# Kernel optimization log

Measured on AMD Instinct MI355X. Metric: run time of the kernel, lower is better.

## Reference

```python
import jax, jax.numpy as jnp
import numpy as np

G = 8192          # graphs in batch
A = 5             # num_agents (nodes per graph)
N = G * A         # total nodes
IN_CH = 29
HID = 64
HEADS = 8
D = HID * HEADS   # 512, node/graph feature dim
NOPT = 4
ADIM = 3


def _lin(key, fan_in, fan_out):
    return jax.random.normal(key, (fan_in, fan_out), jnp.float32) / np.sqrt(fan_in)


def setup_inputs() -> dict:
    key = jax.random.key(0)
    ks = jax.random.split(key, 40)
    # --- graph structure: G fully-connected 5-node graphs + self loops ---
    pairs = np.array([(i, j) for i in range(A) for j in range(A) if i != j])  # [20,2]
    base = (np.arange(G)[:, None] * A)
    src = (base + pairs[None, :, 0]).reshape(-1)
    dst = (base + pairs[None, :, 1]).reshape(-1)
    # GATConv adds self loops (fill_value=0.0 for edge_attr)
    loop = np.arange(N)
    edge_src = jnp.asarray(np.concatenate([src, loop]), jnp.int32)
    edge_dst = jnp.asarray(np.concatenate([dst, loop]), jnp.int32)
    e_real = jax.random.uniform(ks[0], (src.shape[0], 1), jnp.float32)
    edge_attr = jnp.concatenate([e_real, jnp.zeros((N, 1), jnp.float32)], axis=0)
    batch_map = jnp.asarray(np.repeat(np.arange(G), A), jnp.int32)
    x = jax.random.normal(ks[1], (N, IN_CH), jnp.float32)
    sc = 1.0 / np.sqrt(HID)
    inp = dict(
        x=x, edge_attr=edge_attr, edge_src=edge_src, edge_dst=edge_dst, batch_map=batch_map,
        # conv1
        W1=_lin(ks[2], IN_CH, D), as1=jax.random.normal(ks[3], (HEADS, HID)) * sc,
        ad1=jax.random.normal(ks[4], (HEADS, HID)) * sc, We1=_lin(ks[5], 1, D),
        ae1=jax.random.normal(ks[6], (HEADS, HID)) * sc, b1=jnp.zeros((D,), jnp.float32),
        # conv2
        W2=_lin(ks[7], D, D), as2=jax.random.normal(ks[8], (HEADS, HID)) * sc,
        ad2=jax.random.normal(ks[9], (HEADS, HID)) * sc, We2=_lin(ks[10], 1, D),
        ae2=jax.random.normal(ks[11], (HEADS, HID)) * sc, b2=jnp.zeros((D,), jnp.float32),
        # policy-over-options head
        pw1=_lin(ks[12], D, 2 * HID), pb1=jnp.zeros((2 * HID,)), pw2=_lin(ks[13], 2 * HID, NOPT), pb2=jnp.zeros((NOPT,)),
        # q-options head
        qw1=_lin(ks[14], D, 2 * HID), qb1=jnp.zeros((2 * HID,)), qw2=_lin(ks[15], 2 * HID, NOPT), qb2=jnp.zeros((NOPT,)),
        # intra-option actor head (option 0), input dim = node + graph feature = 2*D
        aw1=_lin(ks[16], 2 * D, 2 * HID), ab1=jnp.zeros((2 * HID,)), aw2=_lin(ks[17], 2 * HID, 2 * ADIM), ab2=jnp.zeros((2 * ADIM,)),
        # termination head (option 0)
        tw1=_lin(ks[18], D, HID), tb1=jnp.zeros((HID,)), tw2=_lin(ks[19], HID, 1), tb2=jnp.zeros((1,)),
        action_limits=jnp.array([1.0, 1.0, 3.14159], jnp.float32),
    )
    return inp


def _gat(x, src, dst, eattr, W, a_s, a_d, We, a_e, b):
    n = x.shape[0]
    h = (x @ W).reshape(n, HEADS, HID)                      # [N,H,C]
    e = (eattr @ We).reshape(-1, HEADS, HID)                # [E,H,C]
    lg = ((h * a_s).sum(-1)[src] + (h * a_d).sum(-1)[dst]
          + (e * a_e).sum(-1))                              # [E,H]
    lg = jnp.where(lg > 0, lg, 0.2 * lg)                    # leaky_relu(0.2)
    m = jax.ops.segment_max(lg, dst, num_segments=n)
    p = jnp.exp(lg - m[dst])
    denom = jax.ops.segment_sum(p, dst, num_segments=n)[dst] + 1e-16
    alpha = p / denom                                       # scatter-softmax over dst
    out = jax.ops.segment_sum(alpha[:, :, None] * h[src], dst, num_segments=n)
    return out.reshape(n, HEADS * HID) + b


def reference(x, edge_attr, edge_src, edge_dst, batch_map,
              W1, as1, ad1, We1, ae1, b1,
              W2, as2, ad2, We2, ae2, b2,
              pw1, pb1, pw2, pb2, qw1, qb1, qw2, qb2,
              aw1, ab1, aw2, ab2, tw1, tb1, tw2, tb2, action_limits):
    h = jax.nn.relu(_gat(x, edge_src, edge_dst, edge_attr, W1, as1, ad1, We1, ae1, b1))
    h = jax.nn.relu(_gat(h, edge_src, edge_dst, edge_attr, W2, as2, ad2, We2, ae2, b2))
    # global_mean_pool
    cnt = jax.ops.segment_sum(jnp.ones((h.shape[0],), h.dtype), batch_map, num_segments=G)
    g = jax.ops.segment_sum(h, batch_map, num_segments=G) / cnt[:, None]   # [G,D]
    pi = jax.nn.relu(g @ pw1 + pb1) @ pw2 + pb2                            # [G,NOPT]
    q = jax.nn.relu(g @ qw1 + qb1) @ qw2 + qb2                             # [G,NOPT]
    term = jax.nn.sigmoid(jax.nn.relu(g @ tw1 + tb1) @ tw2 + tb2)          # [G,1]
    # per-graph first num_agents nodes == all nodes here (5 per graph)
    agent = h.reshape(G, A, D)
    comb = jnp.concatenate([agent, jnp.broadcast_to(g[:, None, :], (G, A, D))], axis=-1)
    ho = jax.nn.relu(comb @ aw1 + ab1) @ aw2 + ab2                          # [G,A,6]
    mean_raw, log_std_raw = jnp.split(ho, 2, axis=-1)
    mean = jnp.tanh(mean_raw) * action_limits                               # [G,A,3]
    std = 0.05 + jax.nn.sigmoid(log_std_raw) * 0.45 + 1e-6
    return jnp.concatenate([pi, q, term, mean.reshape(G, -1), std.reshape(G, -1)], axis=1)
```

## Files before the change

kernel.cpp:

```cpp
#include <hip/hip_runtime.h>
#include <hip/hip_bf16.h>
#include <math.h>

#define GG 8192
#define AA 5
#define NN (GG * AA)
#define DD 512

typedef unsigned short ushort_t;
typedef unsigned int uint_t;

__device__ inline float bf2f(ushort_t u) {
  union { uint_t i; float f; } c; c.i = ((uint_t)u) << 16; return c.f;
}
__device__ inline ushort_t f2bf(float f) {
  union { float f; uint_t i; } c; c.f = f;
  uint_t r = c.i + 0x7fffu + ((c.i >> 16) & 1u);
  return (ushort_t)(r >> 16);
}

using frag8 = __attribute__((ext_vector_type(8))) short;
using f32x4 = __attribute__((ext_vector_type(4))) float;

typedef __attribute__((address_space(3))) void lds_void;
typedef __attribute__((address_space(1))) const void gbl_void;
#define GLL(g, l) __builtin_amdgcn_global_load_lds((gbl_void*)(g), (lds_void*)(l), 16, 0, 0)

__device__ inline int xcd_swz(int bid, int nwg) {
  return (bid & 7) * (nwg >> 3) + (bid >> 3);
}

__global__ __launch_bounds__(256) void k_prep(
    const float* __restrict__ x, const float* __restrict__ W1,
    const float* __restrict__ W2, const float* __restrict__ pw1,
    const float* __restrict__ qw1, const float* __restrict__ tw1,
    const float* __restrict__ aw1, const float* __restrict__ pb1,
    const float* __restrict__ qb1, const float* __restrict__ tb1,
    const float* __restrict__ ab1, const float* __restrict__ We1,
    const float* __restrict__ ae1, const float* __restrict__ We2,
    const float* __restrict__ ae2, const float* __restrict__ as1,
    const float* __restrict__ ad1, const float* __restrict__ as2,
    const float* __restrict__ ad2, const float* __restrict__ pw2,
    const float* __restrict__ pb2, const float* __restrict__ qw2,
    const float* __restrict__ qb2, const float* __restrict__ tw2,
    const float* __restrict__ tb2, const float* __restrict__ aw2,
    const float* __restrict__ ab2, ushort_t* __restrict__ xpad32,
    ushort_t* __restrict__ W1T32, ushort_t* __restrict__ W2T,
    ushort_t* __restrict__ WcatT, ushort_t* __restrict__ aw1topT,
    ushort_t* __restrict__ wsc1T, ushort_t* __restrict__ wsc2T,
    float* __restrict__ bcat, float* __restrict__ sce,
    float* __restrict__ woutT, float* __restrict__ bout) {
  int b = blockIdx.x;
  int t = threadIdx.x;
  if (b < 1024) {
    int i = b * 256 + t;
    int n = i >> 9, k = i & 511;
    W2T[(size_t)n * 512 + k] = f2bf(W2[(size_t)k * 512 + n]);
    float v;
    if (n < 128)      v = pw1[(size_t)k * 128 + n];
    else if (n < 256) v = qw1[(size_t)k * 128 + (n - 128)];
    else if (n < 320) v = tw1[(size_t)k * 64 + (n - 256)];
    else if (n < 448) v = aw1[(size_t)(512 + k) * 128 + (n - 320)];
    else              v = 0.f;
    WcatT[(size_t)n * 512 + k] = f2bf(v);
    if (n < 128) aw1topT[(size_t)n * 512 + k] = f2bf(aw1[(size_t)k * 128 + n]);
    if (k == 0) {
      float bv;
      if (n < 128)      bv = pb1[n];
      else if (n < 256) bv = qb1[n - 128];
      else if (n < 320) bv = tb1[n - 256];
      else if (n < 448) bv = ab1[n - 320];
      else              bv = 0.f;
      bcat[n] = bv;
    }
    if (i < 512 * 32) {
      int nn = i >> 5, kk = i & 31;
      W1T32[i] = (kk < 29) ? f2bf(W1[(size_t)kk * 512 + nn]) : (ushort_t)0;
    }
    if (i < 16384) {
      int k2 = i & 511, srow = i >> 9;
      int nh2 = srow >> 4, s = srow & 15;
      float val = 0.f;
      if (s < 8) {
        int head = nh2 * 4 + (s >> 1);
        const float* av = ((s & 1) ? ad2 : as2) + head * 64;
        const float* wr = W2 + (size_t)k2 * 512 + head * 64;
        for (int c = 0; c < 64; ++c) val = fmaf(wr[c], av[c], val);
      }
      wsc2T[i] = f2bf(val);
    }
    if (i < 1024) {
      int k1 = i & 31, srow = i >> 5;
      int nh1 = srow >> 4, s = srow & 15;
      float val = 0.f;
      if (s < 8 && k1 < 29) {
        int head = nh1 * 4 + (s >> 1);
        const float* av = ((s & 1) ? ad1 : as1) + head * 64;
        const float* wr = W1 + (size_t)k1 * 512 + head * 64;
        for (int c = 0; c < 64; ++c) val = fmaf(wr[c], av[c], val);
      }
      wsc1T[i] = f2bf(val);
    }
    if (i < 16) {
      int h = i & 7;
      const float* Wp = (i < 8) ? We1 : We2;
      const float* ap = (i < 8) ? ae1 : ae2;
      float c = 0.f;
      for (int k2 = 0; k2 < 64; ++k2) c = fmaf(Wp[h * 64 + k2], ap[h * 64 + k2], c);
      sce[i] = c;
    }
    if (i < 5120) {
      int j = i / 40, o = i % 40;
      float wv;
      if (o < 4)       wv = pw2[j * 4 + o];
      else if (o < 8)  wv = qw2[j * 4 + (o - 4)];
      else if (o == 8) wv = (j < 64) ? tw2[j] : 0.f;
      else if (o < 24) wv = aw2[j * 6 + (o - 9) % 3];
      else if (o < 39) wv = aw2[j * 6 + 3 + (o - 24) % 3];
      else             wv = 0.f;
      woutT[i] = wv;
      if (j == 0) {
        float bv;
        if (o < 4)       bv = pb2[o];
        else if (o < 8)  bv = qb2[o - 4];
        else if (o == 8) bv = tb2[0];
        else if (o < 24) bv = ab2[(o - 9) % 3];
        else if (o < 39) bv = ab2[3 + (o - 24) % 3];
        else             bv = 0.f;
        bout[o] = bv;
      }
    }
  } else {
    int i = (b - 1024) * 256 + t;
    int n = i >> 5, k = i & 31;
    xpad32[i] = (k < 29) ? f2bf(x[(size_t)n * 29 + k]) : (ushort_t)0;
  }
}

template <int KDIM, bool POOL>
__global__ __launch_bounds__(512) void k_fused(
    const ushort_t* __restrict__ A, const ushort_t* __restrict__ BT,
    const ushort_t* __restrict__ WS, const float* __restrict__ eattr,
    const float* __restrict__ sce, const float* __restrict__ bvec,
    ushort_t* __restrict__ hout, ushort_t* __restrict__ gmean) {
  __shared__ __align__(16) char smem[54016];
  const int t = threadIdx.x;
  const int lane = t & 63;
  const int w = t >> 6;
  const int l15 = lane & 15;
  const int ko2 = ((((lane >> 4) ^ (lane & 3) ^ ((lane >> 2) & 3)) & 3) * 16);
  int lid = xcd_swz(blockIdx.x, gridDim.x);
  const int mb = lid >> 1, nh = lid & 1;
  const int m0 = mb * 80;
  const int g0 = mb * 16;
  const int n0 = nh * 256;
  const ushort_t* WSn = WS + (size_t)nh * 16 * KDIM;
  constexpr int nt = KDIM / 32;
  f32x4 acc[5][2] = {};
  f32x4 asc[5] = {};
  float* sss = (float*)(smem + 45056);
  float* ssd = (float*)(smem + 46336);
  float* sal = (float*)(smem + 47616);
#define FSTAGE(bi, kk0)                                                        \
  {                                                                            \
    char* bb_ = smem + (bi) * 16384;                                           \
    char* aa_ = smem + 32768 + (bi) * 5120;                                    \
    char* sb_ = smem + 43008 + (bi) * 1024;                                    \
    _Pragma("unroll")                                                          \
    for (int r_ = 0; r_ < 2; ++r_) {                                           \
      int c_ = t + r_ * 512; int row_ = c_ >> 2;                               \
      int sw_ = ((((c_ & 3) ^ (row_ & 3) ^ ((row_ >> 2) & 3)) & 3)) * 8;       \
      GLL(BT + (size_t)(n0 + row_) * KDIM + (kk0) + sw_, bb_ + c_ * 16);       \
    }                                                                          \
    if (t < 320) {                                                             \
      int c_ = t; int row_ = c_ >> 2;                                          \
      int sw_ = ((((c_ & 3) ^ (row_ & 3) ^ ((row_ >> 2) & 3)) & 3)) * 8;       \
      GLL(A + (size_t)(m0 + row_) * KDIM + (kk0) + sw_, aa_ + c_ * 16);        \
    } else if (t < 384) {                                                      \
      int c_ = t - 320; int row_ = c_ >> 2;                                    \
      int sw_ = ((((c_ & 3) ^ (row_ & 3) ^ ((row_ >> 2) & 3)) & 3)) * 8;       \
      GLL(WSn + (size_t)row_ * KDIM + (kk0) + sw_, sb_ + c_ * 16);             \
    }                                                                          \
  }
  FSTAGE(0, 0);
  for (int ts = 0; ts < nt; ++ts) {
    int cur = ts & 1;
    if (ts + 1 < nt) {
      FSTAGE(cur ^ 1, (ts + 1) * 32);
      if (w < 6) { asm volatile("s_waitcnt vmcnt(3)" ::: "memory"); }
      else       { asm volatile("s_waitcnt vmcnt(2)" ::: "memory"); }
    } else {
      asm volatile("s_waitcnt vmcnt(0)" ::: "memory");
    }
    __builtin_amdgcn_s_barrier();
    __builtin_amdgcn_sched_barrier(0);
    const char* bb = smem + cur * 16384;
    const char* aa = smem + 32768 + cur * 5120;
    const char* sb = smem + 43008 + cur * 1024;
    frag8 af[5], bfr[2];
#pragma unroll
    for (int mt = 0; mt < 5; ++mt)
      af[mt] = *(const frag8*)(aa + (mt * 16 + l15) * 64 + ko2);
#pragma unroll
    for (int n = 0; n < 2; ++n)
      bfr[n] = *(const frag8*)(bb + ((2 * w + n) * 16 + l15) * 64 + ko2);
    __builtin_amdgcn_s_setprio(1);
#pragma unroll
    for (int mt = 0; mt < 5; ++mt)
#pragma unroll
      for (int n = 0; n < 2; ++n)
        acc[mt][n] = __builtin_amdgcn_mfma_f32_16x16x32_bf16(af[mt], bfr[n], acc[mt][n], 0, 0, 0);
    if (w == 7) {
      frag8 sfr = *(const frag8*)(sb + l15 * 64 + ko2);
#pragma unroll
      for (int mt = 0; mt < 5; ++mt)
        asc[mt] = __builtin_amdgcn_mfma_f32_16x16x32_bf16(af[mt], sfr, asc[mt], 0, 0, 0);
    }
    __builtin_amdgcn_s_setprio(0);
    __builtin_amdgcn_sched_barrier(0);
    if (ts == nt - 1 && w == 7 && l15 < 8) {
      float* dst = (lane & 1) ? ssd : sss;
      int hd = l15 >> 1;
      int q4 = (lane >> 4) * 4;
#pragma unroll
      for (int mt = 0; mt < 5; ++mt)
#pragma unroll
        for (int r = 0; r < 4; ++r)
          dst[(mt * 16 + q4 + r) * 4 + hd] = asc[mt][r];
    }
    __builtin_amdgcn_s_barrier();
  }
#undef FSTAGE
  float* hbf = (float*)smem;
  {
    if (w < 4) {
      int q4 = (lane >> 4) * 4;
#pragma unroll
      for (int mt = 0; mt < 5; ++mt)
#pragma unroll
        for (int n = 0; n < 2; ++n) {
          int lc = w * 32 + n * 16 + l15;
#pragma unroll
          for (int r = 0; r < 4; ++r)
            hbf[(mt * 16 + q4 + r) * 132 + lc] = acc[mt][n][r];
        }
    } else if (t - 256 < 160) {
      int u = t - 256;
      int gi = u / 10, jh = u % 10;
      int j = jh >> 1, hd0 = jh & 1;
#pragma unroll
      for (int hh = 0; hh < 2; ++hh) {
        int hd = hd0 + hh * 2;
        int g = g0 + gi;
        float sdj = ssd[(gi * 5 + j) * 4 + hd];
        float ce = sce[nh * 4 + hd];
        float lg[5], mx = -1e30f;
#pragma unroll
        for (int i = 0; i < 5; ++i) {
          float l = sss[(gi * 5 + i) * 4 + hd] + sdj;
          if (i != j) l = fmaf(eattr[(size_t)g * 20 + i * 4 + (j > i ? j - 1 : j)], ce, l);
          l = l > 0.f ? l : 0.2f * l;
          lg[i] = l; mx = fmaxf(mx, l);
        }
        float s = 0.f;
#pragma unroll
        for (int i = 0; i < 5; ++i) { lg[i] = __expf(lg[i] - mx); s += lg[i]; }
        float inv = 1.f / (s + 1e-16f);
#pragma unroll
        for (int i = 0; i < 5; ++i) sal[((gi * 5 + j) * 5 + i) * 4 + hd] = lg[i] * inv;
      }
    }
  }
  __syncthreads();
#pragma unroll
  for (int half = 0; half < 2; ++half) {
    if (half == 1) {
      if (w >= 4) {
        int q4 = (lane >> 4) * 4;
#pragma unroll
        for (int mt = 0; mt < 5; ++mt)
#pragma unroll
          for (int n = 0; n < 2; ++n) {
            int lc = (w - 4) * 32 + n * 16 + l15;
#pragma unroll
            for (int r = 0; r < 4; ++r)
              hbf[(mt * 16 + q4 + r) * 132 + lc] = acc[mt][n][r];
          }
      }
      __syncthreads();
    }
    int gi = t >> 5, cq = t & 31;
    int hd = half * 2 + (cq >> 4);
    int colg = n0 + half * 128 + cq * 4;
    float hv[5][4];
#pragma unroll
    for (int i = 0; i < 5; ++i)
      *(float4*)hv[i] = *(const float4*)&hbf[(gi * 5 + i) * 132 + cq * 4];
    float4 bb4 = *(const float4*)&bvec[colg];
    float gs0 = 0.f, gs1 = 0.f, gs2 = 0.f, gs3 = 0.f;
#pragma unroll
    for (int j = 0; j < 5; ++j) {
      float o0 = bb4.x, o1 = bb4.y, o2 = bb4.z, o3 = bb4.w;
#pragma unroll
      for (int i = 0; i < 5; ++i) {
        float a = sal[((gi * 5 + j) * 5 + i) * 4 + hd];
        o0 = fmaf(a, hv[i][0], o0); o1 = fmaf(a, hv[i][1], o1);
        o2 = fmaf(a, hv[i][2], o2); o3 = fmaf(a, hv[i][3], o3);
      }
      o0 = fmaxf(o0, 0.f); o1 = fmaxf(o1, 0.f);
      o2 = fmaxf(o2, 0.f); o3 = fmaxf(o3, 0.f);
      uint2 wv_;
      wv_.x = (uint_t)f2bf(o0) | ((uint_t)f2bf(o1) << 16);
      wv_.y = (uint_t)f2bf(o2) | ((uint_t)f2bf(o3) << 16);
      *(uint2*)(hout + ((size_t)(g0 + gi) * 5 + j) * 512 + colg) = wv_;
      if (POOL) { gs0 += o0; gs1 += o1; gs2 += o2; gs3 += o3; }
    }
    if (POOL) {
      uint2 wv_;
      wv_.x = (uint_t)f2bf(gs0 * 0.2f) | ((uint_t)f2bf(gs1 * 0.2f) << 16);
      wv_.y = (uint_t)f2bf(gs2 * 0.2f) | ((uint_t)f2bf(gs3 * 0.2f) << 16);
      *(uint2*)(gmean + (size_t)(g0 + gi) * 512 + colg) = wv_;
    }
    if (half == 0) __syncthreads();
  }
}

template <int EPI>
__device__ __forceinline__ void gemm_body(
    const ushort_t* __restrict__ A, const ushort_t* __restrict__ BT,
    const float* __restrict__ bias, void* __restrict__ Cv,
    int M, int N, int K, int m0, int n0, char* lds) {
  int t = threadIdx.x;
  int lane = t & 63;
  int wv = t >> 6;
  int wr = (wv >> 1) * 64, wc = (wv & 1) * 64;
  f32x4 acc[4][4] = {};
  int ch0 = t, ch1 = t + 256;
  int row0 = ch0 >> 2, row1 = ch1 >> 2;
  int sw0 = (((ch0 & 3) ^ (row0 & 3) ^ ((row0 >> 2) & 3)) & 3) * 8;
  int sw1 = (((ch1 & 3) ^ (row1 & 3) ^ ((row1 >> 2) & 3)) & 3) * 8;
  int ko2 = ((((lane >> 4) ^ (lane & 3) ^ ((lane >> 2) & 3)) & 3) * 16);
  const int nt = K >> 5;
#define STAGE(bi, kk0)                                                         \
  {                                                                            \
    char* ab = lds + (bi) * 16384;                                             \
    GLL(A + (size_t)(m0 + row0) * K + (kk0) + sw0, ab + ch0 * 16);             \
    GLL(A + (size_t)(m0 + row1) * K + (kk0) + sw1, ab + ch1 * 16);             \
    GLL(BT + (size_t)(n0 + row0) * K + (kk0) + sw0, ab + 8192 + ch0 * 16);     \
    GLL(BT + (size_t)(n0 + row1) * K + (kk0) + sw1, ab + 8192 + ch1 * 16);     \
  }
  STAGE(0, 0);
  if (nt > 1) STAGE(1, 32);
  for (int ts = 0; ts < nt; ++ts) {
    int bi = ts % 3;
    if (ts + 2 < nt) {
      STAGE((ts + 2) % 3, (ts + 2) * 32);
      asm volatile("s_waitcnt vmcnt(8)" ::: "memory");
    } else if (ts + 1 < nt) {
      asm volatile("s_waitcnt vmcnt(4)" ::: "memory");
    } else {
      asm volatile("s_waitcnt vmcnt(0)" ::: "memory");
    }
    __builtin_amdgcn_s_barrier();
    __builtin_amdgcn_sched_barrier(0);
    const char* ab = lds + bi * 16384;
    frag8 af[4], bfr[4];
#pragma unroll
    for (int m = 0; m < 4; ++m)
      af[m] = *(const frag8*)(ab + (wr + m * 16 + (lane & 15)) * 64 + ko2);
#pragma unroll
    for (int n = 0; n < 4; ++n)
      bfr[n] = *(const frag8*)(ab + 8192 + (wc + n * 16 + (lane & 15)) * 64 + ko2);
#pragma unroll
    for (int m = 0; m < 4; ++m)
#pragma unroll
      for (int n = 0; n < 4; ++n)
        acc[m][n] = __builtin_amdgcn_mfma_f32_16x16x32_bf16(af[m], bfr[n], acc[m][n], 0, 0, 0);
    __builtin_amdgcn_sched_barrier(0);
    __builtin_amdgcn_s_barrier();
  }
#undef STAGE
  int r4 = (lane >> 4) * 4;
  int cl = lane & 15;
#pragma unroll
  for (int m = 0; m < 4; ++m) {
#pragma unroll
    for (int n = 0; n < 4; ++n) {
      int col = n0 + wc + n * 16 + cl;
      float bb = (EPI == 2) ? bias[col] : 0.f;
#pragma unroll
      for (int r = 0; r < 4; ++r) {
        int row = m0 + wr + m * 16 + r4 + r;
        float v = acc[m][n][r] + bb;
        if (EPI == 2 && col < 320) v = fmaxf(v, 0.f);
        ((float*)Cv)[(size_t)row * N + col] = v;
      }
    }
  }
}

__global__ __launch_bounds__(256) void k_hgemm(
    const ushort_t* __restrict__ h2, const ushort_t* __restrict__ aw1topT,
    float* __restrict__ ahid, const ushort_t* __restrict__ gmean,
    const ushort_t* __restrict__ WcatT, const float* __restrict__ bcat,
    float* __restrict__ hcat) {
  __shared__ char lds[49152];
  int bid = blockIdx.x;
  if (bid < 320) {
    int lid = xcd_swz(bid, 320);
    gemm_body<1>(h2, aw1topT, nullptr, ahid, NN, 128, DD, lid * 128, 0, lds);
  } else {
    int lid = xcd_swz(bid - 320, 256);
    gemm_body<2>(gmean, WcatT, bcat, hcat, GG, DD, DD, (lid >> 2) * 128, (lid & 3) * 128, lds);
  }
}

__global__ __launch_bounds__(256) void k_heads(
    const float* __restrict__ hcat, const float* __restrict__ ahid,
    const float* __restrict__ woutT, const float* __restrict__ bout,
    const float* __restrict__ alim, float* __restrict__ out) {
  int g0 = blockIdx.x * 4;
  int t = threadIdx.x;
  __shared__ float sbuf[4224];
  for (int i = t; i < 4224; i += 256) {
    int gi = i / 1056, r = i - gi * 1056;
    const float* grow = hcat + (size_t)(g0 + gi) * 512;
    float v = 0.f;
    if (r < 128)                  v = grow[r];
    else if (r >= 132 && r < 260) v = grow[128 + r - 132];
    else if (r >= 264 && r < 328) v = grow[256 + r - 264];
    else if (r >= 396) {
      int q = r - 396; int a = q / 132; int j = q - a * 132;
      if (j < 128)
        v = fmaxf(ahid[((size_t)(g0 + gi) * 5 + a) * 128 + j] + grow[320 + j], 0.f);
    }
    sbuf[i] = v;
  }
  __syncthreads();
  int gi = t >> 6, o = t & 63;
  int oc = o < 39 ? o : 39;
  int seg;
  if (oc < 4)       seg = 0;
  else if (oc < 8)  seg = 132;
  else if (oc == 8) seg = 264;
  else {
    int idx = (oc < 24) ? oc - 9 : oc - 24;
    seg = 396 + (idx / 3) * 132;
  }
  const float* ip = &sbuf[gi * 1056 + seg];
  float a0 = 0.f, a1 = 0.f, a2 = 0.f, a3 = 0.f;
#pragma unroll
  for (int j = 0; j < 128; j += 4) {
    a0 = fmaf(ip[j + 0], woutT[(j + 0) * 40 + oc], a0);
    a1 = fmaf(ip[j + 1], woutT[(j + 1) * 40 + oc], a1);
    a2 = fmaf(ip[j + 2], woutT[(j + 2) * 40 + oc], a2);
    a3 = fmaf(ip[j + 3], woutT[(j + 3) * 40 + oc], a3);
  }
  float res = (a0 + a1) + (a2 + a3) + bout[oc];
  if (o < 39) {
    if (o == 8)       res = 1.f / (1.f + __expf(-res));
    else if (o >= 24) res = 0.05f + 0.45f / (1.f + __expf(-res)) + 1e-6f;
    else if (o >= 9)  res = tanhf(res) * alim[(o - 9) % 3];
    out[(size_t)(g0 + gi) * 39 + o] = res;
  }
}

extern "C" void kernel_launch(void* const* d_in, const int* in_sizes, int n_in,
                              void* d_out, int out_size, void* d_ws, size_t ws_size,
                              hipStream_t stream) {
  const float* x     = (const float*)d_in[0];
  const float* eattr = (const float*)d_in[1];
  const float* W1  = (const float*)d_in[5];
  const float* as1 = (const float*)d_in[6];
  const float* ad1 = (const float*)d_in[7];
  const float* We1 = (const float*)d_in[8];
  const float* ae1 = (const float*)d_in[9];
  const float* b1  = (const float*)d_in[10];
  const float* W2  = (const float*)d_in[11];
  const float* as2 = (const float*)d_in[12];
  const float* ad2 = (const float*)d_in[13];
  const float* We2 = (const float*)d_in[14];
  const float* ae2 = (const float*)d_in[15];
  const float* b2  = (const float*)d_in[16];
  const float* pw1 = (const float*)d_in[17];
  const float* pb1 = (const float*)d_in[18];
  const float* pw2 = (const float*)d_in[19];
  const float* pb2 = (const float*)d_in[20];
  const float* qw1 = (const float*)d_in[21];
  const float* qb1 = (const float*)d_in[22];
  const float* qw2 = (const float*)d_in[23];
  const float* qb2 = (const float*)d_in[24];
  const float* aw1 = (const float*)d_in[25];
  const float* ab1 = (const float*)d_in[26];
  const float* aw2 = (const float*)d_in[27];
  const float* ab2 = (const float*)d_in[28];
  const float* tw1 = (const float*)d_in[29];
  const float* tb1 = (const float*)d_in[30];
  const float* tw2 = (const float*)d_in[31];
  const float* tb2 = (const float*)d_in[32];
  const float* alim = (const float*)d_in[33];

  const size_t BIGE = (size_t)NN * DD;
  char* p = (char*)d_ws;
  ushort_t* h1     = (ushort_t*)p; p += BIGE * 2;
  ushort_t* h2     = (ushort_t*)p; p += BIGE * 2;
  ushort_t* gmean  = (ushort_t*)p; p += (size_t)GG * DD * 2;
  ushort_t* xpad32 = (ushort_t*)p; p += (size_t)NN * 32 * 2;
  ushort_t* W1T32  = (ushort_t*)p; p += (size_t)512 * 32 * 2;
  ushort_t* W2T    = (ushort_t*)p; p += (size_t)512 * 512 * 2;
  ushort_t* WcatT  = (ushort_t*)p; p += (size_t)512 * 512 * 2;
  ushort_t* aw1topT = (ushort_t*)p; p += (size_t)128 * 512 * 2;
  ushort_t* wsc1T  = (ushort_t*)p; p += (size_t)2 * 16 * 32 * 2;
  ushort_t* wsc2T  = (ushort_t*)p; p += (size_t)2 * 16 * 512 * 2;
  float* bcat  = (float*)p; p += 512 * 4;
  float* sce   = (float*)p; p += 16 * 4;
  float* woutT = (float*)p; p += 5120 * 4;
  float* bout  = (float*)p; p += 40 * 4;
  float* ahid  = (float*)p; p += (size_t)NN * 128 * 4;
  float* hcat  = (float*)p;

  k_prep<<<1024 + 5120, 256, 0, stream>>>(
      x, W1, W2, pw1, qw1, tw1, aw1, pb1, qb1, tb1, ab1,
      We1, ae1, We2, ae2, as1, ad1, as2, ad2,
      pw2, pb2, qw2, qb2, tw2, tb2, aw2, ab2,
      xpad32, W1T32, W2T, WcatT, aw1topT, wsc1T, wsc2T,
      bcat, sce, woutT, bout);
  k_fused<32, false><<<(NN / 80) * 2, 512, 0, stream>>>(
      xpad32, W1T32, wsc1T, eattr, sce, b1, h1, nullptr);
  k_fused<512, true><<<(NN / 80) * 2, 512, 0, stream>>>(
      h1, W2T, wsc2T, eattr, sce + 8, b2, h2, gmean);
  k_hgemm<<<320 + 256, 256, 0, stream>>>(h2, aw1topT, ahid, gmean, WcatT, bcat, hcat);
  k_heads<<<GG / 4, 256, 0, stream>>>(hcat, ahid, woutT, bout, alim, (float*)d_out);
}
```

Measured before the change: 114.0 us.

## Halve fused GAT block to 4 waves and deepen load pipeline to three stages

```diff
diff --git a/kernel.cpp b/kernel.cpp
--- a/kernel.cpp
+++ b/kernel.cpp
@@ -138,12 +138,12 @@
 }
 
 template <int KDIM, bool POOL>
-__global__ __launch_bounds__(512) void k_fused(
+__global__ __launch_bounds__(256) void k_fused(
     const ushort_t* __restrict__ A, const ushort_t* __restrict__ BT,
     const ushort_t* __restrict__ WS, const float* __restrict__ eattr,
     const float* __restrict__ sce, const float* __restrict__ bvec,
     ushort_t* __restrict__ hout, ushort_t* __restrict__ gmean) {
-  __shared__ __align__(16) char smem[54016];
+  __shared__ __align__(16) char smem[67584];
   const int t = threadIdx.x;
   const int lane = t & 63;
   const int w = t >> 6;
@@ -156,7 +156,7 @@
   const int n0 = nh * 256;
   const ushort_t* WSn = WS + (size_t)nh * 16 * KDIM;
   constexpr int nt = KDIM / 32;
-  f32x4 acc[5][2] = {};
+  f32x4 acc[5][4] = {};
   f32x4 asc[5] = {};
   float* sss = (float*)(smem + 45056);
   float* ssd = (float*)(smem + 46336);
@@ -164,53 +164,59 @@
 #define FSTAGE(bi, kk0)                                                        \
   {                                                                            \
     char* bb_ = smem + (bi) * 16384;                                           \
-    char* aa_ = smem + 32768 + (bi) * 5120;                                    \
-    char* sb_ = smem + 43008 + (bi) * 1024;                                    \
+    char* aa_ = smem + 49152 + (bi) * 5120;                                    \
+    char* sb_ = smem + 64512 + (bi) * 1024;                                    \
     _Pragma("unroll")                                                          \
-    for (int r_ = 0; r_ < 2; ++r_) {                                           \
-      int c_ = t + r_ * 512; int row_ = c_ >> 2;                               \
+    for (int r_ = 0; r_ < 4; ++r_) {                                           \
+      int c_ = t + r_ * 256; int row_ = c_ >> 2;                               \
       int sw_ = ((((c_ & 3) ^ (row_ & 3) ^ ((row_ >> 2) & 3)) & 3)) * 8;       \
       GLL(BT + (size_t)(n0 + row_) * KDIM + (kk0) + sw_, bb_ + c_ * 16);       \
     }                                                                          \
-    if (t < 320) {                                                             \
+    {                                                                          \
       int c_ = t; int row_ = c_ >> 2;                                          \
       int sw_ = ((((c_ & 3) ^ (row_ & 3) ^ ((row_ >> 2) & 3)) & 3)) * 8;       \
       GLL(A + (size_t)(m0 + row_) * KDIM + (kk0) + sw_, aa_ + c_ * 16);        \
-    } else if (t < 384) {                                                      \
-      int c_ = t - 320; int row_ = c_ >> 2;                                    \
+    }                                                                          \
+    if (t < 64) {                                                              \
+      int c_ = t + 256; int row_ = c_ >> 2;                                    \
+      int sw_ = ((((c_ & 3) ^ (row_ & 3) ^ ((row_ >> 2) & 3)) & 3)) * 8;       \
+      GLL(A + (size_t)(m0 + row_) * KDIM + (kk0) + sw_, aa_ + c_ * 16);        \
+    } else if (t < 128) {                                                      \
+      int c_ = t - 64; int row_ = c_ >> 2;                                     \
       int sw_ = ((((c_ & 3) ^ (row_ & 3) ^ ((row_ >> 2) & 3)) & 3)) * 8;       \
       GLL(WSn + (size_t)row_ * KDIM + (kk0) + sw_, sb_ + c_ * 16);             \
     }                                                                          \
   }
   FSTAGE(0, 0);
+  if constexpr (nt > 1) FSTAGE(1, 32);
   for (int ts = 0; ts < nt; ++ts) {
-    int cur = ts & 1;
+    int bi = ts % 3;
     if (ts + 1 < nt) {
-      FSTAGE(cur ^ 1, (ts + 1) * 32);
-      if (w < 6) { asm volatile("s_waitcnt vmcnt(3)" ::: "memory"); }
-      else       { asm volatile("s_waitcnt vmcnt(2)" ::: "memory"); }
+      if (w < 2) { asm volatile("s_waitcnt vmcnt(6)" ::: "memory"); }
+      else       { asm volatile("s_waitcnt vmcnt(5)" ::: "memory"); }
     } else {
       asm volatile("s_waitcnt vmcnt(0)" ::: "memory");
     }
     __builtin_amdgcn_s_barrier();
     __builtin_amdgcn_sched_barrier(0);
-    const char* bb = smem + cur * 16384;
-    const char* aa = smem + 32768 + cur * 5120;
-    const char* sb = smem + 43008 + cur * 1024;
-    frag8 af[5], bfr[2];
+    if (ts + 2 < nt) FSTAGE((ts + 2) % 3, (ts + 2) * 32);
+    const char* bb = smem + bi * 16384;
+    const char* aa = smem + 49152 + bi * 5120;
+    const char* sb = smem + 64512 + bi * 1024;
+    frag8 af[5], bfr[4];
 #pragma unroll
     for (int mt = 0; mt < 5; ++mt)
       af[mt] = *(const frag8*)(aa + (mt * 16 + l15) * 64 + ko2);
 #pragma unroll
-    for (int n = 0; n < 2; ++n)
-      bfr[n] = *(const frag8*)(bb + ((2 * w + n) * 16 + l15) * 64 + ko2);
+    for (int n = 0; n < 4; ++n)
+      bfr[n] = *(const frag8*)(bb + ((4 * w + n) * 16 + l15) * 64 + ko2);
     __builtin_amdgcn_s_setprio(1);
 #pragma unroll
     for (int mt = 0; mt < 5; ++mt)
 #pragma unroll
-      for (int n = 0; n < 2; ++n)
+      for (int n = 0; n < 4; ++n)
         acc[mt][n] = __builtin_amdgcn_mfma_f32_16x16x32_bf16(af[mt], bfr[n], acc[mt][n], 0, 0, 0);
-    if (w == 7) {
+    if (w == 3) {
       frag8 sfr = *(const frag8*)(sb + l15 * 64 + ko2);
 #pragma unroll
       for (int mt = 0; mt < 5; ++mt)
@@ -218,34 +224,33 @@
     }
     __builtin_amdgcn_s_setprio(0);
     __builtin_amdgcn_sched_barrier(0);
-    if (ts == nt - 1 && w == 7 && l15 < 8) {
-      float* dst = (lane & 1) ? ssd : sss;
-      int hd = l15 >> 1;
-      int q4 = (lane >> 4) * 4;
-#pragma unroll
-      for (int mt = 0; mt < 5; ++mt)
+  }
+#undef FSTAGE
+  if (w == 3 && l15 < 8) {
+    float* dst = (lane & 1) ? ssd : sss;
+    int hd = l15 >> 1;
+    int q4 = (lane >> 4) * 4;
+#pragma unroll
+    for (int mt = 0; mt < 5; ++mt)
+#pragma unroll
+      for (int r = 0; r < 4; ++r)
+        dst[(mt * 16 + q4 + r) * 4 + hd] = asc[mt][r];
+  }
+  __syncthreads();
+  float* hbf = (float*)smem;
+  if (w < 2) {
+    int q4 = (lane >> 4) * 4;
+#pragma unroll
+    for (int mt = 0; mt < 5; ++mt)
+#pragma unroll
+      for (int n = 0; n < 4; ++n) {
+        int lc = w * 64 + n * 16 + l15;
 #pragma unroll
         for (int r = 0; r < 4; ++r)
-          dst[(mt * 16 + q4 + r) * 4 + hd] = asc[mt][r];
-    }
-    __builtin_amdgcn_s_barrier();
-  }
-#undef FSTAGE
-  float* hbf = (float*)smem;
-  {
-    if (w < 4) {
-      int q4 = (lane >> 4) * 4;
-#pragma unroll
-      for (int mt = 0; mt < 5; ++mt)
-#pragma unroll
-        for (int n = 0; n < 2; ++n) {
-          int lc = w * 32 + n * 16 + l15;
-#pragma unroll
-          for (int r = 0; r < 4; ++r)
-            hbf[(mt * 16 + q4 + r) * 132 + lc] = acc[mt][n][r];
-        }
-    } else if (t - 256 < 160) {
-      int u = t - 256;
+          hbf[(mt * 16 + q4 + r) * 132 + lc] = acc[mt][n][r];
+      }
+  } else {
+    for (int u = t - 128; u < 160; u += 128) {
       int gi = u / 10, jh = u % 10;
       int j = jh >> 1, hd0 = jh & 1;
 #pragma unroll
@@ -275,13 +280,13 @@
 #pragma unroll
   for (int half = 0; half < 2; ++half) {
     if (half == 1) {
-      if (w >= 4) {
+      if (w >= 2) {
         int q4 = (lane >> 4) * 4;
 #pragma unroll
         for (int mt = 0; mt < 5; ++mt)
 #pragma unroll
-          for (int n = 0; n < 2; ++n) {
-            int lc = (w - 4) * 32 + n * 16 + l15;
+          for (int n = 0; n < 4; ++n) {
+            int lc = (w - 2) * 64 + n * 16 + l15;
 #pragma unroll
             for (int r = 0; r < 4; ++r)
               hbf[(mt * 16 + q4 + r) * 132 + lc] = acc[mt][n][r];
@@ -289,37 +294,41 @@
       }
       __syncthreads();
     }
-    int gi = t >> 5, cq = t & 31;
-    int hd = half * 2 + (cq >> 4);
-    int colg = n0 + half * 128 + cq * 4;
-    float hv[5][4];
-#pragma unroll
-    for (int i = 0; i < 5; ++i)
-      *(float4*)hv[i] = *(const float4*)&hbf[(gi * 5 + i) * 132 + cq * 4];
-    float4 bb4 = *(const float4*)&bvec[colg];
-    float gs0 = 0.f, gs1 = 0.f, gs2 = 0.f, gs3 = 0.f;
-#pragma unroll
-    for (int j = 0; j < 5; ++j) {
-      float o0 = bb4.x, o1 = bb4.y, o2 = bb4.z, o3 = bb4.w;
-#pragma unroll
-      for (int i = 0; i < 5; ++i) {
-        float a = sal[((gi * 5 + j) * 5 + i) * 4 + hd];
-        o0 = fmaf(a, hv[i][0], o0); o1 = fmaf(a, hv[i][1], o1);
-        o2 = fmaf(a, hv[i][2], o2); o3 = fmaf(a, hv[i][3], o3);
-      }
-      o0 = fmaxf(o0, 0.f); o1 = fmaxf(o1, 0.f);
-      o2 = fmaxf(o2, 0.f); o3 = fmaxf(o3, 0.f);
-      uint2 wv_;
-      wv_.x = (uint_t)f2bf(o0) | ((uint_t)f2bf(o1) << 16);
-      wv_.y = (uint_t)f2bf(o2) | ((uint_t)f2bf(o3) << 16);
-      *(uint2*)(hout + ((size_t)(g0 + gi) * 5 + j) * 512 + colg) = wv_;
-      if (POOL) { gs0 += o0; gs1 += o1; gs2 += o2; gs3 += o3; }
-    }
-    if (POOL) {
-      uint2 wv_;
-      wv_.x = (uint_t)f2bf(gs0 * 0.2f) | ((uint_t)f2bf(gs1 * 0.2f) << 16);
-      wv_.y = (uint_t)f2bf(gs2 * 0.2f) | ((uint_t)f2bf(gs3 * 0.2f) << 16);
-      *(uint2*)(gmean + (size_t)(g0 + gi) * 512 + colg) = wv_;
+#pragma unroll
+    for (int uu = 0; uu < 2; ++uu) {
+      int u = t + uu * 256;
+      int gi = u >> 5, cq = u & 31;
+      int hd = half * 2 + (cq >> 4);
+      int colg = n0 + half * 128 + cq * 4;
+      float hv[5][4];
+#pragma unroll
+      for (int i = 0; i < 5; ++i)
+        *(float4*)hv[i] = *(const float4*)&hbf[(gi * 5 + i) * 132 + cq * 4];
+      float4 bb4 = *(const float4*)&bvec[colg];
+      float gs0 = 0.f, gs1 = 0.f, gs2 = 0.f, gs3 = 0.f;
+#pragma unroll
+      for (int j = 0; j < 5; ++j) {
+        float o0 = bb4.x, o1 = bb4.y, o2 = bb4.z, o3 = bb4.w;
+#pragma unroll
+        for (int i = 0; i < 5; ++i) {
+          float a = sal[((gi * 5 + j) * 5 + i) * 4 + hd];
+          o0 = fmaf(a, hv[i][0], o0); o1 = fmaf(a, hv[i][1], o1);
+          o2 = fmaf(a, hv[i][2], o2); o3 = fmaf(a, hv[i][3], o3);
+        }
+        o0 = fmaxf(o0, 0.f); o1 = fmaxf(o1, 0.f);
+        o2 = fmaxf(o2, 0.f); o3 = fmaxf(o3, 0.f);
+        uint2 wv_;
+        wv_.x = (uint_t)f2bf(o0) | ((uint_t)f2bf(o1) << 16);
+        wv_.y = (uint_t)f2bf(o2) | ((uint_t)f2bf(o3) << 16);
+        *(uint2*)(hout + ((size_t)(g0 + gi) * 5 + j) * 512 + colg) = wv_;
+        if (POOL) { gs0 += o0; gs1 += o1; gs2 += o2; gs3 += o3; }
+      }
+      if (POOL) {
+        uint2 wv_;
+        wv_.x = (uint_t)f2bf(gs0 * 0.2f) | ((uint_t)f2bf(gs1 * 0.2f) << 16);
+        wv_.y = (uint_t)f2bf(gs2 * 0.2f) | ((uint_t)f2bf(gs3 * 0.2f) << 16);
+        *(uint2*)(gmean + (size_t)(g0 + gi) * 512 + colg) = wv_;
+      }
     }
     if (half == 0) __syncthreads();
   }
@@ -525,9 +534,9 @@
       pw2, pb2, qw2, qb2, tw2, tb2, aw2, ab2,
       xpad32, W1T32, W2T, WcatT, aw1topT, wsc1T, wsc2T,
       bcat, sce, woutT, bout);
-  k_fused<32, false><<<(NN / 80) * 2, 512, 0, stream>>>(
+  k_fused<32, false><<<(NN / 80) * 2, 256, 0, stream>>>(
       xpad32, W1T32, wsc1T, eattr, sce, b1, h1, nullptr);
-  k_fused<512, true><<<(NN / 80) * 2, 512, 0, stream>>>(
+  k_fused<512, true><<<(NN / 80) * 2, 256, 0, stream>>>(
       h1, W2T, wsc2T, eattr, sce + 8, b2, h2, gmean);
   k_hgemm<<<320 + 256, 256, 0, stream>>>(h2, aw1topT, ahid, gmean, WcatT, bcat, hcat);
   k_heads<<<GG / 4, 256, 0, stream>>>(hcat, ahid, woutT, bout, alim, (float*)d_out);
```

Measured after the change: 146.2 us. 28.2% more time.
